# Kernel tuning notes

Measured on AMD Instinct MI355X. Metric: run time of the kernel, lower is better.

## Reference

```python
import jax, jax.numpy as jnp
import numpy as np

LEVELS = 256
# round(d*cos(a)), round(d*sin(a)) for d=1, angles 0, pi/4, pi/2, 3pi/4 (torch defaults)
SHIFTS = [(1, 0), (1, 1), (0, 1), (-1, 1)]


def _glcm(gray):
    # gray: (n, h, w) int32 in [0, LEVELS-1]
    n = gray.shape[0]
    B = LEVELS * LEVELS
    cooc = []
    for dx, dy in SHIFTS:  # fixed small set of angles
        shifted = jnp.roll(gray, shift=(dx, dy), axis=(1, 2))
        joint = (gray * LEVELS + shifted).reshape(n, -1)  # (n, h*w)
        vmin = joint.min()
        vmax = joint.max()
        # faithful torch.histc binning: B equal-width bins over [vmin, vmax],
        # values == vmax fall in last bin (handled by clip)
        scale = B / jnp.maximum((vmax - vmin).astype(jnp.float32), 1.0)
        bins = jnp.clip(
            jnp.floor((joint - vmin).astype(jnp.float32) * scale).astype(jnp.int32),
            0, B - 1)
        bidx = jnp.broadcast_to(jnp.arange(n)[:, None], joint.shape)
        hist = jnp.zeros((n, B), jnp.float32).at[bidx, bins].add(1.0)
        cooc.append(hist.reshape(n, LEVELS, LEVELS).sum(axis=0))
    co = jnp.stack(cooc, axis=-1)            # (L, L, A)
    co = co + jnp.swapaxes(co, 0, 1)          # symmetric=True
    glcm = co / co.sum()                      # normalize over ALL dims incl. angles (as torch)
    return glcm[:, :, None, :]                # (L, L, n_dist=1, A)


def _contrast(glcm):
    i = jnp.arange(LEVELS, dtype=jnp.float32)
    w = (i[:, None] - i[None, :]) ** 2        # (L, L) contrast weights
    return jnp.sum(glcm * w[:, :, None, None], axis=(0, 1))  # (n_dist, A)


def _loss(original, generated):
    og = jax.lax.stop_gradient(
        jnp.round(original.mean(axis=1) * (LEVELS - 1)).astype(jnp.int32))
    gg = jax.lax.stop_gradient(
        jnp.round(generated.mean(axis=1) * (LEVELS - 1)).astype(jnp.int32))
    return jnp.mean(jnp.abs(_contrast(_glcm(og)) - _contrast(_glcm(gg))))


def setup_inputs() -> dict:
    key = jax.random.key(0)
    k1, k2 = jax.random.split(key)
    shape = (16, 3, 512, 512)
    return {
        "original": jax.random.uniform(k1, shape, dtype=jnp.float32),
        "generated": jax.random.uniform(k2, shape, dtype=jnp.float32),
    }


def reference(original, generated):
    return _loss(original, generated)
```

## Files before the change

kernel.cpp:

```cpp
#include <hip/hip_runtime.h>

#define W 512
#define NPIX 4194304

union Bytes { uint4 v; unsigned char b[16]; };

__device__ __forceinline__ unsigned char gray1(float a, float b, float c) {
    return (unsigned char)__float2int_rn(((a + b + c) / 3.0f) * 255.0f);
}

__global__ __launch_bounds__(256, 4) void k1_gray_minmax(
    const float4* __restrict__ og, const float4* __restrict__ gg,
    uchar4* __restrict__ gray, unsigned int* __restrict__ blockmm) {
    int inp = blockIdx.y;
    int img = blockIdx.x >> 5;
    int r0 = (blockIdx.x & 31) << 4;
    const float4* src = (inp ? gg : og) + (size_t)img * 3 * 65536;
    uchar4* gout = gray + (size_t)inp * (NPIX / 4) + img * 65536;
    const float4* s0 = src;
    const float4* s1 = src + 65536;
    const float4* s2 = src + 131072;

    __shared__ unsigned char lds[18 * W];
    uchar4* lds4 = (uchar4*)lds;

    int off[9];
#pragma unroll
    for (int j = 0; j < 9; ++j) {
        int q = threadIdx.x + j * 256;
        int i = q >> 7, quad = q & 127;
        int ir = (r0 - 1 + i) & 511;
        off[j] = ir * 128 + quad;
    }
    float4 a = s0[off[0]], b = s1[off[0]], c = s2[off[0]];
#pragma unroll
    for (int j = 0; j < 9; ++j) {
        float4 an, bn, cn;
        if (j < 8) { an = s0[off[j + 1]]; bn = s1[off[j + 1]]; cn = s2[off[j + 1]]; }
        uchar4 r;
        r.x = gray1(a.x, b.x, c.x);
        r.y = gray1(a.y, b.y, c.y);
        r.z = gray1(a.z, b.z, c.z);
        r.w = gray1(a.w, b.w, c.w);
        lds4[threadIdx.x + j * 256] = r;
        int i = (threadIdx.x + j * 256) >> 7;
        if (i >= 1 && i <= 16) gout[off[j]] = r;
        a = an; b = bn; c = cn;
    }
    __syncthreads();

    int lr = 1 + (threadIdx.x >> 4);
    int c0 = (threadIdx.x & 15) << 5;
    const unsigned char* Lm = lds + (lr - 1) * W;
    const unsigned char* Lc = lds + lr * W;
    const unsigned char* Lp = lds + (lr + 1) * W;
    Bytes rm[2], rc[2], rp[2];
    rm[0].v = *(const uint4*)(Lm + c0); rm[1].v = *(const uint4*)(Lm + c0 + 16);
    rc[0].v = *(const uint4*)(Lc + c0); rc[1].v = *(const uint4*)(Lc + c0 + 16);
    rp[0].v = *(const uint4*)(Lp + c0); rp[1].v = *(const uint4*)(Lp + c0 + 16);
    int cp = (c0 - 1) & 511;
    unsigned char pm = Lm[cp], pc = Lc[cp], pp = Lp[cp];

    unsigned int lmin[4] = {~0u, ~0u, ~0u, ~0u};
    unsigned int lmax[4] = {0u, 0u, 0u, 0u};
#pragma unroll
    for (int h = 0; h < 2; ++h) {
#pragma unroll
        for (int j = 0; j < 16; ++j) {
            unsigned int base = ((unsigned int)rc[h].b[j]) << 8;
            unsigned int v0 = base + rm[h].b[j];
            unsigned int v1 = base + (j ? rm[h].b[j - 1] : (h ? rm[0].b[15] : pm));
            unsigned int v2 = base + (j ? rc[h].b[j - 1] : (h ? rc[0].b[15] : pc));
            unsigned int v3 = base + (j ? rp[h].b[j - 1] : (h ? rp[0].b[15] : pp));
            lmin[0] = min(lmin[0], v0); lmax[0] = max(lmax[0], v0);
            lmin[1] = min(lmin[1], v1); lmax[1] = max(lmax[1], v1);
            lmin[2] = min(lmin[2], v2); lmax[2] = max(lmax[2], v2);
            lmin[3] = min(lmin[3], v3); lmax[3] = max(lmax[3], v3);
        }
    }
#pragma unroll
    for (int off2 = 32; off2 > 0; off2 >>= 1) {
#pragma unroll
        for (int s = 0; s < 4; ++s) {
            lmin[s] = min(lmin[s], (unsigned int)__shfl_down((int)lmin[s], off2));
            lmax[s] = max(lmax[s], (unsigned int)__shfl_down((int)lmax[s], off2));
        }
    }
    __shared__ unsigned int wmin[4][4], wmax[4][4];
    int wave = threadIdx.x >> 6;
    if ((threadIdx.x & 63) == 0) {
#pragma unroll
        for (int s = 0; s < 4; ++s) { wmin[wave][s] = lmin[s]; wmax[wave][s] = lmax[s]; }
    }
    __syncthreads();
    if (threadIdx.x < 4) {
        int s = threadIdx.x;
        unsigned int mn = min(min(wmin[0][s], wmin[1][s]), min(wmin[2][s], wmin[3][s]));
        unsigned int mx = max(max(wmax[0][s], wmax[1][s]), max(wmax[2][s], wmax[3][s]));
        blockmm[inp * 4096 + s * 512 + blockIdx.x] = mn;
        blockmm[inp * 4096 + (4 + s) * 512 + blockIdx.x] = mx;
    }
}

__global__ __launch_bounds__(256, 4) void k2_contrast(
    const uchar4* __restrict__ gray, const unsigned int* __restrict__ blockmm,
    unsigned int* __restrict__ partial) {
    int inp = blockIdx.y;
    int img = blockIdx.x >> 5;
    int r0 = (blockIdx.x & 31) << 4;

    __shared__ unsigned char lds[18 * W];
    __shared__ unsigned int mmfin[8];
    uchar4* lds4 = (uchar4*)lds;
    const uchar4* gin = gray + (size_t)inp * (NPIX / 4) + img * 65536;

    int off[9];
#pragma unroll
    for (int j = 0; j < 9; ++j) {
        int q = threadIdx.x + j * 256;
        int i = q >> 7, quad = q & 127;
        int ir = (r0 - 1 + i) & 511;
        off[j] = ir * 128 + quad;
    }
    uchar4 g0 = gin[off[0]];
#pragma unroll
    for (int j = 0; j < 9; ++j) {
        uchar4 gn;
        if (j < 8) gn = gin[off[j + 1]];
        lds4[threadIdx.x + j * 256] = g0;
        g0 = gn;
    }
    {
        int s8 = threadIdx.x >> 5, lane = threadIdx.x & 31;
        const unsigned int* mb = blockmm + inp * 4096 + s8 * 512;
        unsigned int v = mb[lane];
#pragma unroll
        for (int k = 1; k < 16; ++k) {
            unsigned int u = mb[lane + k * 32];
            v = (s8 < 4) ? min(v, u) : max(v, u);
        }
#pragma unroll
        for (int off2 = 16; off2 > 0; off2 >>= 1) {
            unsigned int u = (unsigned int)__shfl_down((int)v, off2, 32);
            v = (s8 < 4) ? min(v, u) : max(v, u);
        }
        if (lane == 0) mmfin[s8] = v;
    }
    __syncthreads();

    unsigned int vm[4]; float scale[4];
#pragma unroll
    for (int s = 0; s < 4; ++s) {
        vm[s] = mmfin[s];
        scale[s] = 65536.0f / fmaxf((float)(mmfin[4 + s] - vm[s]), 1.0f);
    }

    int lr = 1 + (threadIdx.x >> 4);
    int c0 = (threadIdx.x & 15) << 5;
    const unsigned char* Lm = lds + (lr - 1) * W;
    const unsigned char* Lc = lds + lr * W;
    const unsigned char* Lp = lds + (lr + 1) * W;
    Bytes rm[2], rc[2], rp[2];
    rm[0].v = *(const uint4*)(Lm + c0); rm[1].v = *(const uint4*)(Lm + c0 + 16);
    rc[0].v = *(const uint4*)(Lc + c0); rc[1].v = *(const uint4*)(Lc + c0 + 16);
    rp[0].v = *(const uint4*)(Lp + c0); rp[1].v = *(const uint4*)(Lp + c0 + 16);
    int cp = (c0 - 1) & 511;
    unsigned char pm = Lm[cp], pc = Lc[cp], pp = Lp[cp];

    unsigned int acc[4] = {0u, 0u, 0u, 0u};
#pragma unroll
    for (int h = 0; h < 2; ++h) {
#pragma unroll
        for (int j = 0; j < 16; ++j) {
            unsigned int base = ((unsigned int)rc[h].b[j]) << 8;
            unsigned int v[4];
            v[0] = base + rm[h].b[j];
            v[1] = base + (j ? rm[h].b[j - 1] : (h ? rm[0].b[15] : pm));
            v[2] = base + (j ? rc[h].b[j - 1] : (h ? rc[0].b[15] : pc));
            v[3] = base + (j ? rp[h].b[j - 1] : (h ? rp[0].b[15] : pp));
#pragma unroll
            for (int s = 0; s < 4; ++s) {
                int b = (int)((float)(v[s] - vm[s]) * scale[s]);
                b = b > 65535 ? 65535 : b;
                int d = (b >> 8) - (b & 255);
                acc[s] += (unsigned int)(d * d);
            }
        }
    }
#pragma unroll
    for (int off2 = 32; off2 > 0; off2 >>= 1)
#pragma unroll
        for (int s = 0; s < 4; ++s)
            acc[s] += (unsigned int)__shfl_down((int)acc[s], off2);

    __shared__ unsigned int wsum[4][4];
    int wave = threadIdx.x >> 6;
    if ((threadIdx.x & 63) == 0) {
#pragma unroll
        for (int s = 0; s < 4; ++s) wsum[wave][s] = acc[s];
    }
    __syncthreads();
    if (threadIdx.x < 4) {
        int s = threadIdx.x;
        unsigned int tot = wsum[0][s] + wsum[1][s] + wsum[2][s] + wsum[3][s];
        partial[(inp * 4 + s) * 512 + blockIdx.x] = tot;
    }
}

__global__ __launch_bounds__(256) void k3_loss(
    const unsigned int* __restrict__ partial, float* __restrict__ out) {
    int c = threadIdx.x >> 5;
    int lane = threadIdx.x & 31;
    const unsigned int* p = partial + c * 512;
    double acc = 0.0;
#pragma unroll
    for (int k = 0; k < 16; ++k) acc += (double)p[lane + k * 32];
#pragma unroll
    for (int off = 16; off > 0; off >>= 1) acc += __shfl_down(acc, off, 32);
    __shared__ double cs[8];
    if (lane == 0) cs[c] = acc;
    __syncthreads();
    if (threadIdx.x == 0) {
        double r = 0.0;
        for (int a = 0; a < 4; ++a) {
            double co = 2.0 * cs[a]     / 33554432.0;
            double cg = 2.0 * cs[4 + a] / 33554432.0;
            r += fabs(co - cg);
        }
        out[0] = (float)(r * 0.25);
    }
}

extern "C" void kernel_launch(void* const* d_in, const int* in_sizes, int n_in,
                              void* d_out, int out_size, void* d_ws, size_t ws_size,
                              hipStream_t stream) {
    const float4* og = (const float4*)d_in[0];
    const float4* gg = (const float4*)d_in[1];
    float* out = (float*)d_out;

    unsigned int* blockmm = (unsigned int*)d_ws;
    unsigned int* partial = blockmm + 8192;
    uchar4* gray = (uchar4*)((char*)d_ws + 65536);

    dim3 grid(512, 2);
    k1_gray_minmax<<<grid, 256, 0, stream>>>(og, gg, gray, blockmm);
    k2_contrast<<<grid, 256, 0, stream>>>(gray, blockmm, partial);
    k3_loss<<<1, 256, 0, stream>>>(partial, out);
}
```

Before: 40.62 us.

## Drop LDS staging in contrast kernel, load neighbours directly from global per thread

The contrast kernel no longer copies an 18-row tile into shared memory. Each thread now handles 16 pixels instead of 32 and reads its three neighbour rows straight from global memory (which stays hot in L2). The grid doubles to 1024 blocks per input with higher occupancy bounds, and the final reduction reads twice as many partials. This removes the LDS fill and its barrier but reloads each row three times from cache.

Result: no change. 40.86 us (+0.6%).

```diff
diff --git a/kernel.cpp b/kernel.cpp
--- a/kernel.cpp
+++ b/kernel.cpp
@@ -102,34 +102,29 @@
     }
 }
 
-__global__ __launch_bounds__(256, 4) void k2_contrast(
-    const uchar4* __restrict__ gray, const unsigned int* __restrict__ blockmm,
+__global__ __launch_bounds__(256, 8) void k2_contrast(
+    const unsigned char* __restrict__ gray,
+    const unsigned int* __restrict__ blockmm,
     unsigned int* __restrict__ partial) {
     int inp = blockIdx.y;
-    int img = blockIdx.x >> 5;
-    int r0 = (blockIdx.x & 31) << 4;
-
-    __shared__ unsigned char lds[18 * W];
+    const unsigned char* g = gray + (size_t)inp * NPIX;
+    int t = blockIdx.x * 256 + threadIdx.x;
+    int img = t >> 14;
+    int p = t & 16383;
+    int r = p >> 5;
+    int c0 = (p & 31) << 4;
+    const unsigned char* gn = g + (img << 18);
+    int rm1 = (r - 1) & 511, rp1 = (r + 1) & 511, cp = (c0 - 1) & 511;
+
+    Bytes rm, rc, rp;
+    rm.v = *(const uint4*)(gn + (rm1 << 9) + c0);
+    rc.v = *(const uint4*)(gn + (r   << 9) + c0);
+    rp.v = *(const uint4*)(gn + (rp1 << 9) + c0);
+    unsigned char pm = gn[(rm1 << 9) | cp];
+    unsigned char pc = gn[(r   << 9) | cp];
+    unsigned char pp = gn[(rp1 << 9) | cp];
+
     __shared__ unsigned int mmfin[8];
-    uchar4* lds4 = (uchar4*)lds;
-    const uchar4* gin = gray + (size_t)inp * (NPIX / 4) + img * 65536;
-
-    int off[9];
-#pragma unroll
-    for (int j = 0; j < 9; ++j) {
-        int q = threadIdx.x + j * 256;
-        int i = q >> 7, quad = q & 127;
-        int ir = (r0 - 1 + i) & 511;
-        off[j] = ir * 128 + quad;
-    }
-    uchar4 g0 = gin[off[0]];
-#pragma unroll
-    for (int j = 0; j < 9; ++j) {
-        uchar4 gn;
-        if (j < 8) gn = gin[off[j + 1]];
-        lds4[threadIdx.x + j * 256] = g0;
-        g0 = gn;
-    }
     {
         int s8 = threadIdx.x >> 5, lane = threadIdx.x & 31;
         const unsigned int* mb = blockmm + inp * 4096 + s8 * 512;
@@ -140,8 +135,8 @@
             v = (s8 < 4) ? min(v, u) : max(v, u);
         }
 #pragma unroll
-        for (int off2 = 16; off2 > 0; off2 >>= 1) {
-            unsigned int u = (unsigned int)__shfl_down((int)v, off2, 32);
+        for (int off = 16; off > 0; off >>= 1) {
+            unsigned int u = (unsigned int)__shfl_down((int)v, off, 32);
             v = (s8 < 4) ? min(v, u) : max(v, u);
         }
         if (lane == 0) mmfin[s8] = v;
@@ -155,43 +150,28 @@
         scale[s] = 65536.0f / fmaxf((float)(mmfin[4 + s] - vm[s]), 1.0f);
     }
 
-    int lr = 1 + (threadIdx.x >> 4);
-    int c0 = (threadIdx.x & 15) << 5;
-    const unsigned char* Lm = lds + (lr - 1) * W;
-    const unsigned char* Lc = lds + lr * W;
-    const unsigned char* Lp = lds + (lr + 1) * W;
-    Bytes rm[2], rc[2], rp[2];
-    rm[0].v = *(const uint4*)(Lm + c0); rm[1].v = *(const uint4*)(Lm + c0 + 16);
-    rc[0].v = *(const uint4*)(Lc + c0); rc[1].v = *(const uint4*)(Lc + c0 + 16);
-    rp[0].v = *(const uint4*)(Lp + c0); rp[1].v = *(const uint4*)(Lp + c0 + 16);
-    int cp = (c0 - 1) & 511;
-    unsigned char pm = Lm[cp], pc = Lc[cp], pp = Lp[cp];
-
     unsigned int acc[4] = {0u, 0u, 0u, 0u};
 #pragma unroll
-    for (int h = 0; h < 2; ++h) {
-#pragma unroll
-        for (int j = 0; j < 16; ++j) {
-            unsigned int base = ((unsigned int)rc[h].b[j]) << 8;
-            unsigned int v[4];
-            v[0] = base + rm[h].b[j];
-            v[1] = base + (j ? rm[h].b[j - 1] : (h ? rm[0].b[15] : pm));
-            v[2] = base + (j ? rc[h].b[j - 1] : (h ? rc[0].b[15] : pc));
-            v[3] = base + (j ? rp[h].b[j - 1] : (h ? rp[0].b[15] : pp));
-#pragma unroll
-            for (int s = 0; s < 4; ++s) {
-                int b = (int)((float)(v[s] - vm[s]) * scale[s]);
-                b = b > 65535 ? 65535 : b;
-                int d = (b >> 8) - (b & 255);
-                acc[s] += (unsigned int)(d * d);
-            }
-        }
-    }
-#pragma unroll
-    for (int off2 = 32; off2 > 0; off2 >>= 1)
+    for (int j = 0; j < 16; ++j) {
+        unsigned int base = ((unsigned int)rc.b[j]) << 8;
+        unsigned int v[4];
+        v[0] = base + rm.b[j];
+        v[1] = base + (j ? rm.b[j - 1] : pm);
+        v[2] = base + (j ? rc.b[j - 1] : pc);
+        v[3] = base + (j ? rp.b[j - 1] : pp);
+#pragma unroll
+        for (int s = 0; s < 4; ++s) {
+            int b = (int)((float)(v[s] - vm[s]) * scale[s]);
+            b = b > 65535 ? 65535 : b;
+            int d = (b >> 8) - (b & 255);
+            acc[s] += (unsigned int)(d * d);
+        }
+    }
+#pragma unroll
+    for (int off = 32; off > 0; off >>= 1)
 #pragma unroll
         for (int s = 0; s < 4; ++s)
-            acc[s] += (unsigned int)__shfl_down((int)acc[s], off2);
+            acc[s] += (unsigned int)__shfl_down((int)acc[s], off);
 
     __shared__ unsigned int wsum[4][4];
     int wave = threadIdx.x >> 6;
@@ -203,7 +183,7 @@
     if (threadIdx.x < 4) {
         int s = threadIdx.x;
         unsigned int tot = wsum[0][s] + wsum[1][s] + wsum[2][s] + wsum[3][s];
-        partial[(inp * 4 + s) * 512 + blockIdx.x] = tot;
+        partial[(inp * 4 + s) * 1024 + blockIdx.x] = tot;
     }
 }
 
@@ -211,10 +191,10 @@
     const unsigned int* __restrict__ partial, float* __restrict__ out) {
     int c = threadIdx.x >> 5;
     int lane = threadIdx.x & 31;
-    const unsigned int* p = partial + c * 512;
+    const unsigned int* p = partial + c * 1024;
     double acc = 0.0;
 #pragma unroll
-    for (int k = 0; k < 16; ++k) acc += (double)p[lane + k * 32];
+    for (int k = 0; k < 32; ++k) acc += (double)p[lane + k * 32];
 #pragma unroll
     for (int off = 16; off > 0; off >>= 1) acc += __shfl_down(acc, off, 32);
     __shared__ double cs[8];
@@ -240,10 +220,11 @@
 
     unsigned int* blockmm = (unsigned int*)d_ws;
     unsigned int* partial = blockmm + 8192;
-    uchar4* gray = (uchar4*)((char*)d_ws + 65536);
-
-    dim3 grid(512, 2);
-    k1_gray_minmax<<<grid, 256, 0, stream>>>(og, gg, gray, blockmm);
-    k2_contrast<<<grid, 256, 0, stream>>>(gray, blockmm, partial);
+    unsigned char* gray = (unsigned char*)d_ws + 65536;
+
+    dim3 g1(512, 2);
+    k1_gray_minmax<<<g1, 256, 0, stream>>>(og, gg, (uchar4*)gray, blockmm);
+    dim3 g2(1024, 2);
+    k2_contrast<<<g2, 256, 0, stream>>>(gray, blockmm, partial);
     k3_loss<<<1, 256, 0, stream>>>(partial, out);
 }
```
